# Optimization experiments

Measured on AMD Instinct MI355X. Metric: run time of the kernel, lower is better.

## Reference

```python
import jax, jax.numpy as jnp
import numpy as np

N_NODES = 100000
N_EDGES = 1600000
D_IN = 128
D_HID = 256
D_OUT = 128


def _glorot(key, shape):
    fan_in, fan_out = shape[1], shape[0]
    lim = (6.0 / (fan_in + fan_out)) ** 0.5
    return jax.random.uniform(key, shape, jnp.float32, -lim, lim)


def setup_inputs() -> dict:
    key = jax.random.key(0)
    ks = jax.random.split(key, 8)
    x = jax.random.normal(ks[0], (N_NODES, D_IN), jnp.float32)
    edge_index = jax.random.randint(ks[1], (2, N_EDGES), 0, N_NODES, jnp.int32)
    return {
        "x": x,
        "edge_index": edge_index,
        # layer 1: in=D_IN -> D_HID
        "Wl1": _glorot(ks[2], (D_HID, D_IN)), "bl1": jnp.zeros((D_HID,), jnp.float32),
        "Wr1": _glorot(ks[3], (D_HID, D_IN)),
        # layer 2: D_HID -> D_HID
        "Wl2": _glorot(ks[4], (D_HID, D_HID)), "bl2": jnp.zeros((D_HID,), jnp.float32),
        "Wr2": _glorot(ks[5], (D_HID, D_HID)),
        # layer 3: D_HID -> D_OUT
        "Wl3": _glorot(ks[6], (D_OUT, D_HID)), "bl3": jnp.zeros((D_OUT,), jnp.float32),
        "Wr3": _glorot(ks[7], (D_OUT, D_HID)),
    }


def _sage_conv(x, src, dst, inv_deg, Wl, bl, Wr):
    # PyG SAGEConv (aggr='mean'): out = lin_l(mean_j x_j) + lin_r(x_i)
    agg = jax.ops.segment_sum(x[src], dst, num_segments=N_NODES)  # [N, F]
    mean = agg * inv_deg[:, None]
    return mean @ Wl.T + bl + x @ Wr.T


def reference(x, edge_index, Wl1, bl1, Wr1, Wl2, bl2, Wr2, Wl3, bl3, Wr3):
    src, dst = edge_index[0], edge_index[1]
    deg = jax.ops.segment_sum(jnp.ones((src.shape[0],), jnp.float32), dst,
                              num_segments=N_NODES)
    inv_deg = jnp.where(deg > 0, 1.0 / jnp.maximum(deg, 1.0), 0.0)
    h = jax.nn.relu(_sage_conv(x, src, dst, inv_deg, Wl1, bl1, Wr1))
    h = jax.nn.relu(_sage_conv(h, src, dst, inv_deg, Wl2, bl2, Wr2))
    return _sage_conv(h, src, dst, inv_deg, Wl3, bl3, Wr3)
```

## Files before the change

kernel.cpp:

```cpp
#include <hip/hip_runtime.h>

#define NN 100000
#define NE 1600000
#define DIN 128
#define DHID 256
#define DOUT 128
#define CAP 64

typedef unsigned int u32;
typedef unsigned short u16;

typedef __bf16 bf16x8 __attribute__((ext_vector_type(8)));
typedef float  f32x4  __attribute__((ext_vector_type(4)));

__device__ inline u16 f2bf(float f) {
    u32 u = __float_as_uint(f);
    u32 r = u + 0x7FFFu + ((u >> 16) & 1u);
    return (u16)(r >> 16);
}
__device__ inline u32 pack2(float a, float b) {
    return (u32)f2bf(a) | ((u32)f2bf(b) << 16);
}
__device__ inline float bflo(u32 u) { return __uint_as_float(u << 16); }
__device__ inline float bfhi(u32 u) { return __uint_as_float(u & 0xffff0000u); }

__global__ void csr_build(const int* __restrict__ src, const int* __restrict__ dst,
                          int* __restrict__ fill, int* __restrict__ csrC, int nE) {
    int g  = blockIdx.x & 7;
    int bg = blockIdx.x >> 3;
    int nbg = gridDim.x >> 3;
    int lo = g * (NN / 8), hi = lo + (NN / 8);
    for (int e = bg * 256 + threadIdx.x; e < nE; e += nbg * 256) {
        int d = dst[e];
        if (d >= lo && d < hi) {
            int pos = atomicAdd(&fill[d], 1);
            if (pos < CAP) csrC[(size_t)d * CAP + pos] = src[e];
        }
    }
}

__global__ void invdeg_from_fill(const int* __restrict__ fill, float* __restrict__ invdeg, int n) {
    int i = blockIdx.x * 256 + threadIdx.x;
    if (i < n) { int d = fill[i]; invdeg[i] = d > 0 ? 1.0f / (float)d : 0.0f; }
}

__global__ void f32_to_bf16(const float4* __restrict__ in, uint2* __restrict__ outp, int total4) {
    int i = blockIdx.x * 256 + threadIdx.x;
    if (i < total4) {
        float4 v = in[i];
        uint2 r; r.x = pack2(v.x, v.y); r.y = pack2(v.z, v.w);
        outp[i] = r;
    }
}

template<int SH, int OFF>
__global__ __launch_bounds__(256)
void agg_bf16(const u32* __restrict__ feat,
              const int* __restrict__ fill, const float* __restrict__ invdeg,
              const int* __restrict__ csrC, u32* __restrict__ aggOut) {
    int w = (blockIdx.x * 256 + threadIdx.x) >> 6;
    int lane = threadIdx.x & 63;
    if (w >= NN) return;
    int dg = fill[w]; if (dg > CAP) dg = CAP;
    const int* cp = csrC + (size_t)w * CAP;
    float ax0 = 0.f, ay0 = 0.f, ax1 = 0.f, ay1 = 0.f;
    int j = 0;
    for (; j + 3 < dg; j += 4) {
        int s0 = cp[j], s1 = cp[j + 1], s2 = cp[j + 2], s3 = cp[j + 3];
        u32 u0 = feat[((size_t)s0 << SH) + OFF + lane];
        u32 u1 = feat[((size_t)s1 << SH) + OFF + lane];
        u32 u2 = feat[((size_t)s2 << SH) + OFF + lane];
        u32 u3 = feat[((size_t)s3 << SH) + OFF + lane];
        ax0 += bflo(u0) + bflo(u1); ay0 += bfhi(u0) + bfhi(u1);
        ax1 += bflo(u2) + bflo(u3); ay1 += bfhi(u2) + bfhi(u3);
    }
    for (; j < dg; ++j) {
        u32 u0 = feat[((size_t)cp[j] << SH) + OFF + lane];
        ax0 += bflo(u0); ay0 += bfhi(u0);
    }
    float iv = invdeg[w];
    aggOut[(size_t)w * 64 + lane] = pack2((ax0 + ax1) * iv, (ay0 + ay1) * iv);
}

#define TM 128
#define TN 128
#define TK 32
#define LDSTR 40

template<int AF32>
__device__ inline void mfma_pass(const void* __restrict__ A, int K, int lda,
                                 const float* __restrict__ W, int ldw,
                                 int brow, int bcol, int n,
                                 int tid, int lane, int wr, int wc,
                                 u16* As, u16* Ws, f32x4 (&acc)[4][4])
{
    int rsel = lane & 15;
    int krun = (lane >> 4) << 3;
    for (int kt = 0; kt < K; kt += TK) {
        __syncthreads();
#pragma unroll
        for (int it = 0; it < 2; ++it) {
            int c = tid + it * 256;
            int r = c >> 2;
            int k8 = (c & 3) << 3;
            uint4 av = make_uint4(0u, 0u, 0u, 0u);
            int grow = brow + r;
            if (grow < n) {
                if (AF32) {
                    const float* gp = (const float*)A + (size_t)grow * lda + kt + k8;
                    float4 v0 = *(const float4*)gp;
                    float4 v1 = *(const float4*)(gp + 4);
                    av = make_uint4(pack2(v0.x, v0.y), pack2(v0.z, v0.w),
                                    pack2(v1.x, v1.y), pack2(v1.z, v1.w));
                } else {
                    av = *(const uint4*)((const u16*)A + (size_t)grow * lda + kt + k8);
                }
            }
            *(uint4*)&As[r * LDSTR + k8] = av;
            const float* wp = W + (size_t)(bcol + r) * ldw + kt + k8;
            float4 w0 = *(const float4*)wp;
            float4 w1 = *(const float4*)(wp + 4);
            *(uint4*)&Ws[r * LDSTR + k8] =
                make_uint4(pack2(w0.x, w0.y), pack2(w0.z, w0.w),
                           pack2(w1.x, w1.y), pack2(w1.z, w1.w));
        }
        __syncthreads();
        bf16x8 a[4], b[4];
#pragma unroll
        for (int mb = 0; mb < 4; ++mb)
            a[mb] = *(const bf16x8*)&As[(64 * wr + 16 * mb + rsel) * LDSTR + krun];
#pragma unroll
        for (int nb = 0; nb < 4; ++nb)
            b[nb] = *(const bf16x8*)&Ws[(64 * wc + 16 * nb + rsel) * LDSTR + krun];
#pragma unroll
        for (int mb = 0; mb < 4; ++mb)
#pragma unroll
            for (int nb = 0; nb < 4; ++nb)
                acc[mb][nb] = __builtin_amdgcn_mfma_f32_16x16x32_bf16(
                    a[mb], b[nb], acc[mb][nb], 0, 0, 0);
    }
}

template<int A1F32, int A2F32, int CF32, int RELU, int ACCUM>
__global__ __launch_bounds__(256)
void gemm_mfma(const void* __restrict__ A1, int K1, int lda1,
               const float* __restrict__ W1, int ldw1,
               const void* __restrict__ A2, int K2, int lda2,
               const float* __restrict__ W2, int ldw2,
               const float* __restrict__ bias, const u16* __restrict__ accBuf,
               void* __restrict__ C, int n, int cout)
{
    __shared__ u16 As[TM * LDSTR];
    __shared__ u16 Ws[TN * LDSTR];
    int tid = threadIdx.x;
    int lane = tid & 63, wid = tid >> 6;
    int wr = wid >> 1, wc = wid & 1;
    int brow = blockIdx.x * TM, bcol = blockIdx.y * TN;

    f32x4 acc[4][4];
#pragma unroll
    for (int i = 0; i < 4; ++i)
#pragma unroll
        for (int j = 0; j < 4; ++j) acc[i][j] = (f32x4){0.f, 0.f, 0.f, 0.f};

    mfma_pass<A1F32>(A1, K1, lda1, W1, ldw1, brow, bcol, n, tid, lane, wr, wc, As, Ws, acc);
    if (K2 > 0)
        mfma_pass<A2F32>(A2, K2, lda2, W2, ldw2, brow, bcol, n, tid, lane, wr, wc, As, Ws, acc);

    int rsel = lane & 15;
    int rgrp = (lane >> 4) << 2;
    float bv[4];
#pragma unroll
    for (int nb = 0; nb < 4; ++nb)
        bv[nb] = bias ? bias[bcol + 64 * wc + 16 * nb + rsel] : 0.f;

#pragma unroll
    for (int mb = 0; mb < 4; ++mb) {
        int rowb = brow + 64 * wr + 16 * mb + rgrp;
#pragma unroll
        for (int r = 0; r < 4; ++r) {
            int row = rowb + r;
            if (row >= n) continue;
            size_t rof = (size_t)row * cout;
#pragma unroll
            for (int nb = 0; nb < 4; ++nb) {
                int col = bcol + 64 * wc + 16 * nb + rsel;
                float v = acc[mb][nb][r] + bv[nb];
                if (ACCUM == 2) v += __uint_as_float(((u32)accBuf[rof + col]) << 16);
                if (CF32) {
                    float* p = (float*)C + rof + col;
                    if (ACCUM == 1) v += *p;
                    if (RELU) v = fmaxf(v, 0.f);
                    *p = v;
                } else {
                    u16* p = (u16*)C + rof + col;
                    if (ACCUM == 1) v += __uint_as_float(((u32)(*p)) << 16);
                    if (RELU) v = fmaxf(v, 0.f);
                    *p = f2bf(v);
                }
            }
        }
    }
}

extern "C" void kernel_launch(void* const* d_in, const int* in_sizes, int n_in,
                              void* d_out, int out_size, void* d_ws, size_t ws_size,
                              hipStream_t stream) {
    const float* x   = (const float*)d_in[0];
    const int*   ei  = (const int*)d_in[1];
    const float* Wl1 = (const float*)d_in[2];
    const float* bl1 = (const float*)d_in[3];
    const float* Wr1 = (const float*)d_in[4];
    const float* Wl2 = (const float*)d_in[5];
    const float* bl2 = (const float*)d_in[6];
    const float* Wr2 = (const float*)d_in[7];
    const float* Wl3 = (const float*)d_in[8];
    const float* bl3 = (const float*)d_in[9];
    const float* Wr3 = (const float*)d_in[10];
    float* out = (float*)d_out;

    const int* src = ei;
    const int* dst = ei + NE;

    char* ws = (char*)d_ws;
    int*   fill   = (int*)  (ws + 0);
    float* invdeg = (float*)(ws + 400000);
    int*   csrC   = (int*)  (ws + 800000);
    u16*   aggS   = (u16*)  (ws + 26400128);
    u16*   h2     = (u16*)  (ws + 52000128);
    u16*   h1     = (u16*)  (ws + 103200128);
    u16*   x_bf   = h2;
    u16*   t3     = h1;

    dim3 b256(256);
    dim3 gN((NN + 255) / 256);
    dim3 gC((NN * 32 + 255) / 256);
    dim3 gW((NN * 64 + 255) / 256);
    dim3 gg2((NN + TM - 1) / TM, DHID / TN);
    dim3 gg1((NN + TM - 1) / TM, DOUT / TN);

    hipMemsetAsync(fill, 0, 400000, stream);
    hipLaunchKernelGGL(csr_build, dim3(2048), b256, 0, stream, src, dst, fill, csrC, NE);
    hipLaunchKernelGGL(invdeg_from_fill, gN, b256, 0, stream, fill, invdeg, NN);

    hipLaunchKernelGGL(f32_to_bf16, gC, b256, 0, stream,
                       (const float4*)x, (uint2*)x_bf, NN * 32);

    hipLaunchKernelGGL((agg_bf16<6, 0>), gW, b256, 0, stream,
                       (const u32*)x_bf, fill, invdeg, csrC, (u32*)aggS);
    hipLaunchKernelGGL((gemm_mfma<0, 0, 0, 1, 0>), gg2, b256, 0, stream,
                       aggS, DIN, DIN, Wl1, DIN,
                       x_bf, DIN, DIN, Wr1, DIN,
                       bl1, nullptr, h1, NN, DHID);

    hipLaunchKernelGGL((agg_bf16<7, 0>), gW, b256, 0, stream,
                       (const u32*)h1, fill, invdeg, csrC, (u32*)aggS);
    hipLaunchKernelGGL((gemm_mfma<0, 0, 0, 0, 0>), gg2, b256, 0, stream,
                       aggS, 128, 128, Wl2, DHID,
                       h1, DHID, DHID, Wr2, DHID,
                       bl2, nullptr, h2, NN, DHID);
    hipLaunchKernelGGL((agg_bf16<7, 64>), gW, b256, 0, stream,
                       (const u32*)h1, fill, invdeg, csrC, (u32*)aggS);
    hipLaunchKernelGGL((gemm_mfma<0, 0, 0, 1, 1>), gg2, b256, 0, stream,
                       aggS, 128, 128, Wl2 + 128, DHID,
                       nullptr, 0, 0, nullptr, 0,
                       nullptr, nullptr, h2, NN, DHID);

    hipLaunchKernelGGL((gemm_mfma<0, 0, 0, 0, 0>), gg1, b256, 0, stream,
                       h2, DHID, DHID, Wl3, DHID,
                       nullptr, 0, 0, nullptr, 0,
                       nullptr, nullptr, t3, NN, DOUT);
    hipLaunchKernelGGL((agg_bf16<6, 0>), gW, b256, 0, stream,
                       (const u32*)t3, fill, invdeg, csrC, (u32*)aggS);
    hipLaunchKernelGGL((gemm_mfma<0, 0, 1, 0, 2>), gg1, b256, 0, stream,
                       h2, DHID, DHID, Wr3, DHID,
                       nullptr, 0, 0, nullptr, 0,
                       bl3, aggS, out, NN, DOUT);
}
```

Baseline: 589.8 us.

## Build compact CSR with row pointers, prefetch GEMM tiles, pre-convert weights to bf16

Replaces the fixed-capacity padded adjacency (64 slots per node) with a compact CSR built from a degree count, an atomic row-offset allocation and a fill pass. This removes the degree cap and shrinks the adjacency footprint, at the cost of extra kernel launches and a second memset. Weights are converted to bf16 once up front so GEMM tiles load bf16 directly. The GEMM main loop now register-prefetches the next K tile while computing the current one. The aggregation loop is unrolled to 8 neighbours with more independent accumulators.

After: 620.7 us. 5.2% more time.

```diff
diff --git a/kernel.cpp b/kernel.cpp
--- a/kernel.cpp
+++ b/kernel.cpp
@@ -5,7 +5,6 @@
 #define DIN 128
 #define DHID 256
 #define DOUT 128
-#define CAP 64
 
 typedef unsigned int u32;
 typedef unsigned short u16;
@@ -24,8 +23,24 @@
 __device__ inline float bflo(u32 u) { return __uint_as_float(u << 16); }
 __device__ inline float bfhi(u32 u) { return __uint_as_float(u & 0xffff0000u); }
 
-__global__ void csr_build(const int* __restrict__ src, const int* __restrict__ dst,
-                          int* __restrict__ fill, int* __restrict__ csrC, int nE) {
+__global__ void deg_count(const int* __restrict__ dst, int* __restrict__ fill, int nE) {
+    int i = blockIdx.x * 256 + threadIdx.x;
+    if (i < nE) atomicAdd(&fill[dst[i]], 1);
+}
+
+__global__ void alloc_rows(const int* __restrict__ fill, int* __restrict__ rowptr,
+                           float* __restrict__ invdeg, int* __restrict__ gcount, int n) {
+    int i = blockIdx.x * 256 + threadIdx.x;
+    if (i < n) {
+        int d = fill[i];
+        invdeg[i] = d > 0 ? 1.0f / (float)d : 0.0f;
+        rowptr[i] = atomicAdd(gcount, d);
+    }
+}
+
+__global__ void fill_csr_part(const int* __restrict__ src, const int* __restrict__ dst,
+                              const int* __restrict__ rowptr, int* __restrict__ fill,
+                              int* __restrict__ csr, int nE) {
     int g  = blockIdx.x & 7;
     int bg = blockIdx.x >> 3;
     int nbg = gridDim.x >> 3;
@@ -34,14 +49,9 @@
         int d = dst[e];
         if (d >= lo && d < hi) {
             int pos = atomicAdd(&fill[d], 1);
-            if (pos < CAP) csrC[(size_t)d * CAP + pos] = src[e];
+            csr[rowptr[d] + pos] = src[e];
         }
     }
-}
-
-__global__ void invdeg_from_fill(const int* __restrict__ fill, float* __restrict__ invdeg, int n) {
-    int i = blockIdx.x * 256 + threadIdx.x;
-    if (i < n) { int d = fill[i]; invdeg[i] = d > 0 ? 1.0f / (float)d : 0.0f; }
 }
 
 __global__ void f32_to_bf16(const float4* __restrict__ in, uint2* __restrict__ outp, int total4) {
@@ -56,30 +66,47 @@
 template<int SH, int OFF>
 __global__ __launch_bounds__(256)
 void agg_bf16(const u32* __restrict__ feat,
-              const int* __restrict__ fill, const float* __restrict__ invdeg,
-              const int* __restrict__ csrC, u32* __restrict__ aggOut) {
+              const int* __restrict__ rowptr, const int* __restrict__ fill,
+              const float* __restrict__ invdeg, const int* __restrict__ csr,
+              u32* __restrict__ aggOut) {
     int w = (blockIdx.x * 256 + threadIdx.x) >> 6;
     int lane = threadIdx.x & 63;
     if (w >= NN) return;
-    int dg = fill[w]; if (dg > CAP) dg = CAP;
-    const int* cp = csrC + (size_t)w * CAP;
-    float ax0 = 0.f, ay0 = 0.f, ax1 = 0.f, ay1 = 0.f;
+    int dg = fill[w];
+    const int* cp = csr + rowptr[w];
+    float a0 = 0.f, b0 = 0.f, a1 = 0.f, b1 = 0.f;
+    float a2 = 0.f, b2 = 0.f, a3 = 0.f, b3 = 0.f;
     int j = 0;
-    for (; j + 3 < dg; j += 4) {
-        int s0 = cp[j], s1 = cp[j + 1], s2 = cp[j + 2], s3 = cp[j + 3];
+    for (; j + 7 < dg; j += 8) {
+        int s0 = cp[j], s1 = cp[j+1], s2 = cp[j+2], s3 = cp[j+3];
+        int s4 = cp[j+4], s5 = cp[j+5], s6 = cp[j+6], s7 = cp[j+7];
         u32 u0 = feat[((size_t)s0 << SH) + OFF + lane];
         u32 u1 = feat[((size_t)s1 << SH) + OFF + lane];
         u32 u2 = feat[((size_t)s2 << SH) + OFF + lane];
         u32 u3 = feat[((size_t)s3 << SH) + OFF + lane];
-        ax0 += bflo(u0) + bflo(u1); ay0 += bfhi(u0) + bfhi(u1);
-        ax1 += bflo(u2) + bflo(u3); ay1 += bfhi(u2) + bfhi(u3);
-    }
-    for (; j < dg; ++j) {
+        u32 u4 = feat[((size_t)s4 << SH) + OFF + lane];
+        u32 u5 = feat[((size_t)s5 << SH) + OFF + lane];
+        u32 u6 = feat[((size_t)s6 << SH) + OFF + lane];
+        u32 u7 = feat[((size_t)s7 << SH) + OFF + lane];
+        a0 += bflo(u0) + bflo(u1); b0 += bfhi(u0) + bfhi(u1);
+        a1 += bflo(u2) + bflo(u3); b1 += bfhi(u2) + bfhi(u3);
+        a2 += bflo(u4) + bflo(u5); b2 += bfhi(u4) + bfhi(u5);
+        a3 += bflo(u6) + bflo(u7); b3 += bfhi(u6) + bfhi(u7);
+    }
+    for (; j + 1 < dg; j += 2) {
+        int s0 = cp[j], s1 = cp[j+1];
+        u32 u0 = feat[((size_t)s0 << SH) + OFF + lane];
+        u32 u1 = feat[((size_t)s1 << SH) + OFF + lane];
+        a0 += bflo(u0); b0 += bfhi(u0);
+        a1 += bflo(u1); b1 += bfhi(u1);
+    }
+    if (j < dg) {
         u32 u0 = feat[((size_t)cp[j] << SH) + OFF + lane];
-        ax0 += bflo(u0); ay0 += bfhi(u0);
+        a0 += bflo(u0); b0 += bfhi(u0);
     }
     float iv = invdeg[w];
-    aggOut[(size_t)w * 64 + lane] = pack2((ax0 + ax1) * iv, (ay0 + ay1) * iv);
+    aggOut[(size_t)w * 64 + lane] = pack2((a0 + a1 + a2 + a3) * iv,
+                                          (b0 + b1 + b2 + b3) * iv);
 }
 
 #define TM 128
@@ -87,44 +114,40 @@
 #define TK 32
 #define LDSTR 40
 
-template<int AF32>
-__device__ inline void mfma_pass(const void* __restrict__ A, int K, int lda,
-                                 const float* __restrict__ W, int ldw,
-                                 int brow, int bcol, int n,
-                                 int tid, int lane, int wr, int wc,
-                                 u16* As, u16* Ws, f32x4 (&acc)[4][4])
+__device__ inline void mfma_pass_bf(const u16* __restrict__ A, int K, int lda,
+                                    const u16* __restrict__ Wb, int ldw,
+                                    int brow, int bcol, int n,
+                                    int tid, int lane, int wr, int wc,
+                                    u16* As, u16* Ws, f32x4 (&acc)[4][4])
 {
     int rsel = lane & 15;
     int krun = (lane >> 4) << 3;
+    int r0 = tid >> 2,        k80 = (tid & 3) << 3;
+    int r1 = (tid + 256) >> 2, k81 = k80;
+    uint4 av0, av1, wv0, wv1;
+    const uint4 zero4 = make_uint4(0u, 0u, 0u, 0u);
+
+    {
+        int kt = 0;
+        av0 = (brow + r0 < n) ? *(const uint4*)(A + (size_t)(brow + r0) * lda + kt + k80) : zero4;
+        av1 = (brow + r1 < n) ? *(const uint4*)(A + (size_t)(brow + r1) * lda + kt + k81) : zero4;
+        wv0 = *(const uint4*)(Wb + (size_t)(bcol + r0) * ldw + kt + k80);
+        wv1 = *(const uint4*)(Wb + (size_t)(bcol + r1) * ldw + kt + k81);
+    }
     for (int kt = 0; kt < K; kt += TK) {
         __syncthreads();
-#pragma unroll
-        for (int it = 0; it < 2; ++it) {
-            int c = tid + it * 256;
-            int r = c >> 2;
-            int k8 = (c & 3) << 3;
-            uint4 av = make_uint4(0u, 0u, 0u, 0u);
-            int grow = brow + r;
-            if (grow < n) {
-                if (AF32) {
-                    const float* gp = (const float*)A + (size_t)grow * lda + kt + k8;
-                    float4 v0 = *(const float4*)gp;
-                    float4 v1 = *(const float4*)(gp + 4);
-                    av = make_uint4(pack2(v0.x, v0.y), pack2(v0.z, v0.w),
-                                    pack2(v1.x, v1.y), pack2(v1.z, v1.w));
-                } else {
-                    av = *(const uint4*)((const u16*)A + (size_t)grow * lda + kt + k8);
-                }
-            }
-            *(uint4*)&As[r * LDSTR + k8] = av;
-            const float* wp = W + (size_t)(bcol + r) * ldw + kt + k8;
-            float4 w0 = *(const float4*)wp;
-            float4 w1 = *(const float4*)(wp + 4);
-            *(uint4*)&Ws[r * LDSTR + k8] =
-                make_uint4(pack2(w0.x, w0.y), pack2(w0.z, w0.w),
-                           pack2(w1.x, w1.y), pack2(w1.z, w1.w));
+        *(uint4*)&As[r0 * LDSTR + k80] = av0;
+        *(uint4*)&As[r1 * LDSTR + k81] = av1;
+        *(uint4*)&Ws[r0 * LDSTR + k80] = wv0;
+        *(uint4*)&Ws[r1 * LDSTR + k81] = wv1;
+        __syncthreads();
+        int kn = kt + TK;
+        if (kn < K) {
+            av0 = (brow + r0 < n) ? *(const uint4*)(A + (size_t)(brow + r0) * lda + kn + k80) : zero4;
+            av1 = (brow + r1 < n) ? *(const uint4*)(A + (size_t)(brow + r1) * lda + kn + k81) : zero4;
+            wv0 = *(const uint4*)(Wb + (size_t)(bcol + r0) * ldw + kn + k80);
+            wv1 = *(const uint4*)(Wb + (size_t)(bcol + r1) * ldw + kn + k81);
         }
-        __syncthreads();
         bf16x8 a[4], b[4];
 #pragma unroll
         for (int mb = 0; mb < 4; ++mb)
@@ -141,12 +164,12 @@
     }
 }
 
-template<int A1F32, int A2F32, int CF32, int RELU, int ACCUM>
+template<int CF32, int RELU, int ACCUM>
 __global__ __launch_bounds__(256)
-void gemm_mfma(const void* __restrict__ A1, int K1, int lda1,
-               const float* __restrict__ W1, int ldw1,
-               const void* __restrict__ A2, int K2, int lda2,
-               const float* __restrict__ W2, int ldw2,
+void gemm_mfma(const u16* __restrict__ A1, int K1, int lda1,
+               const u16* __restrict__ W1, int ldw1,
+               const u16* __restrict__ A2, int K2, int lda2,
+               const u16* __restrict__ W2, int ldw2,
                const float* __restrict__ bias, const u16* __restrict__ accBuf,
                void* __restrict__ C, int n, int cout)
 {
@@ -163,9 +186,9 @@
 #pragma unroll
         for (int j = 0; j < 4; ++j) acc[i][j] = (f32x4){0.f, 0.f, 0.f, 0.f};
 
-    mfma_pass<A1F32>(A1, K1, lda1, W1, ldw1, brow, bcol, n, tid, lane, wr, wc, As, Ws, acc);
+    mfma_pass_bf(A1, K1, lda1, W1, ldw1, brow, bcol, n, tid, lane, wr, wc, As, Ws, acc);
     if (K2 > 0)
-        mfma_pass<A2F32>(A2, K2, lda2, W2, ldw2, brow, bcol, n, tid, lane, wr, wc, As, Ws, acc);
+        mfma_pass_bf(A2, K2, lda2, W2, ldw2, brow, bcol, n, tid, lane, wr, wc, As, Ws, acc);
 
     int rsel = lane & 15;
     int rgrp = (lane >> 4) << 2;
@@ -224,56 +247,77 @@
 
     char* ws = (char*)d_ws;
     int*   fill   = (int*)  (ws + 0);
-    float* invdeg = (float*)(ws + 400000);
-    int*   csrC   = (int*)  (ws + 800000);
-    u16*   aggS   = (u16*)  (ws + 26400128);
-    u16*   h2     = (u16*)  (ws + 52000128);
-    u16*   h1     = (u16*)  (ws + 103200128);
+    int*   rowptr = (int*)  (ws + 400000);
+    float* invdeg = (float*)(ws + 800000);
+    int*   gcount = (int*)  (ws + 1200000);
+    u16*   Wb     = (u16*)  (ws + 1200064);
+    int*   csr    = (int*)  (ws + 1724416);
+    u16*   aggS   = (u16*)  (ws + 8124544);
+    u16*   h2     = (u16*)  (ws + 33724544);
+    u16*   h1     = (u16*)  (ws + 84924544);
     u16*   x_bf   = h2;
     u16*   t3     = h1;
 
+    u16* wbL1 = Wb + 0;
+    u16* wbR1 = Wb + 32768;
+    u16* wbL2 = Wb + 65536;
+    u16* wbR2 = Wb + 131072;
+    u16* wbL3 = Wb + 196608;
+    u16* wbR3 = Wb + 229376;
+
     dim3 b256(256);
+    dim3 gE((NE + 255) / 256);
     dim3 gN((NN + 255) / 256);
     dim3 gC((NN * 32 + 255) / 256);
     dim3 gW((NN * 64 + 255) / 256);
     dim3 gg2((NN + TM - 1) / TM, DHID / TN);
     dim3 gg1((NN + TM - 1) / TM, DOUT / TN);
 
+    hipLaunchKernelGGL(f32_to_bf16, dim3(32), b256, 0, stream, (const float4*)Wl1, (uint2*)wbL1, 8192);
+    hipLaunchKernelGGL(f32_to_bf16, dim3(32), b256, 0, stream, (const float4*)Wr1, (uint2*)wbR1, 8192);
+    hipLaunchKernelGGL(f32_to_bf16, dim3(64), b256, 0, stream, (const float4*)Wl2, (uint2*)wbL2, 16384);
+    hipLaunchKernelGGL(f32_to_bf16, dim3(64), b256, 0, stream, (const float4*)Wr2, (uint2*)wbR2, 16384);
+    hipLaunchKernelGGL(f32_to_bf16, dim3(32), b256, 0, stream, (const float4*)Wl3, (uint2*)wbL3, 8192);
+    hipLaunchKernelGGL(f32_to_bf16, dim3(32), b256, 0, stream, (const float4*)Wr3, (uint2*)wbR3, 8192);
+
     hipMemsetAsync(fill, 0, 400000, stream);
-    hipLaunchKernelGGL(csr_build, dim3(2048), b256, 0, stream, src, dst, fill, csrC, NE);
-    hipLaunchKernelGGL(invdeg_from_fill, gN, b256, 0, stream, fill, invdeg, NN);
+    hipMemsetAsync(gcount, 0, 64, stream);
+    hipLaunchKernelGGL(deg_count, gE, b256, 0, stream, dst, fill, NE);
+    hipLaunchKernelGGL(alloc_rows, gN, b256, 0, stream, fill, rowptr, invdeg, gcount, NN);
+    hipMemsetAsync(fill, 0, 400000, stream);
+    hipLaunchKernelGGL(fill_csr_part, dim3(2048), b256, 0, stream, src, dst, rowptr, fill, csr, NE);
 
     hipLaunchKernelGGL(f32_to_bf16, gC, b256, 0, stream,
                        (const float4*)x, (uint2*)x_bf, NN * 32);
 
     hipLaunchKernelGGL((agg_bf16<6, 0>), gW, b256, 0, stream,
-                       (const u32*)x_bf, fill, invdeg, csrC, (u32*)aggS);
-    hipLaunchKernelGGL((gemm_mfma<0, 0, 0, 1, 0>), gg2, b256, 0, stream,
-                       aggS, DIN, DIN, Wl1, DIN,
-                       x_bf, DIN, DIN, Wr1, DIN,
+                       (const u32*)x_bf, rowptr, fill, invdeg, csr, (u32*)aggS);
+    hipLaunchKernelGGL((gemm_mfma<0, 1, 0>), gg2, b256, 0, stream,
+                       aggS, DIN, DIN, wbL1, DIN,
+                       x_bf, DIN, DIN, wbR1, DIN,
                        bl1, nullptr, h1, NN, DHID);
 
     hipLaunchKernelGGL((agg_bf16<7, 0>), gW, b256, 0, stream,
-                       (const u32*)h1, fill, invdeg, csrC, (u32*)aggS);
-    hipLaunchKernelGGL((gemm_mfma<0, 0, 0, 0, 0>), gg2, b256, 0, stream,
-                       aggS, 128, 128, Wl2, DHID,
-                       h1, DHID, DHID, Wr2, DHID,
+                       (const u32*)h1, rowptr, fill, invdeg, csr, (u32*)aggS);
+    hipLaunchKernelGGL((gemm_mfma<0, 0, 0>), gg2, b256, 0, stream,
+                       aggS, 128, 128, wbL2, DHID,
+                       h1, DHID, DHID, wbR2, DHID,
                        bl2, nullptr, h2, NN, DHID);
     hipLaunchKernelGGL((agg_bf16<7, 64>), gW, b256, 0, stream,
-                       (const u32*)h1, fill, invdeg, csrC, (u32*)aggS);
-    hipLaunchKernelGGL((gemm_mfma<0, 0, 0, 1, 1>), gg2, b256, 0, stream,
-                       aggS, 128, 128, Wl2 + 128, DHID,
+                       (const u32*)h1, rowptr, fill, invdeg, csr, (u32*)aggS);
+    hipLaunchKernelGGL((gemm_mfma<0, 1, 1>), gg2, b256, 0, stream,
+                       aggS, 128, 128, wbL2 + 128, DHID,
                        nullptr, 0, 0, nullptr, 0,
                        nullptr, nullptr, h2, NN, DHID);
 
-    hipLaunchKernelGGL((gemm_mfma<0, 0, 0, 0, 0>), gg1, b256, 0, stream,
-                       h2, DHID, DHID, Wl3, DHID,
+    hipLaunchKernelGGL((gemm_mfma<0, 0, 0>), gg1, b256, 0, stream,
+                       h2, DHID, DHID, wbL3, DHID,
                        nullptr, 0, 0, nullptr, 0,
                        nullptr, nullptr, t3, NN, DOUT);
     hipLaunchKernelGGL((agg_bf16<6, 0>), gW, b256, 0, stream,
-                       (const u32*)t3, fill, invdeg, csrC, (u32*)aggS);
-    hipLaunchKernelGGL((gemm_mfma<0, 0, 1, 0, 2>), gg1, b256, 0, stream,
-                       h2, DHID, DHID, Wr3, DHID,
+                       (const u32*)t3, rowptr, fill, invdeg, csr, (u32*)aggS);
+    hipLaunchKernelGGL((gemm_mfma<1, 0, 2>), gg1, b256, 0, stream,
+                       h2, DHID, DHID, wbR3, DHID,
                        nullptr, 0, 0, nullptr, 0,
                        bl3, aggS, out, NN, DOUT);
 }
```
